# Kernel tuning notes

Measured on AMD Instinct MI355X. Metric: run time of the kernel, lower is better.

Reference implementation:

```python
import jax, jax.numpy as jnp
import numpy as np

B, N, C, T, K = 32, 4096, 768, 1000, 20

def setup_inputs() -> dict:
    key = jax.random.key(0)
    k1, k2, k3, k4 = jax.random.split(key, 4)
    g_feat = jax.random.normal(k1, (B, 1, C), dtype=jnp.float32)
    inp = jax.random.normal(k2, (B, N, C), dtype=jnp.float32)
    tau = jax.random.uniform(k3, (1,), dtype=jnp.float32)
    text_embeddings = jax.random.normal(k4, (T, C), dtype=jnp.float32) * 0.01
    return {"g_feat": g_feat, "input": inp, "tau": tau, "text_embeddings": text_embeddings}


def reference(g_feat, input, tau, text_embeddings):
    feat = input  # [B, N, C]
    # 1x1 conv of global feature against text embeddings -> class logits [B, T]
    vg_logit = jnp.einsum('bc,tc->bt', g_feat[:, 0, :], text_embeddings)
    # top-20 candidate categories per image
    _, indices = jax.lax.top_k(vg_logit, K)              # [B, K]
    agg_text_features = text_embeddings[indices]          # [B, K, C] gather
    # per-pixel logits against the 20 gathered text embeddings
    seg_logit = jnp.exp(tau[0]) * jnp.einsum('bkc,bnc->bkn', agg_text_features, feat)  # [B, K, N]
    # hard (straight-through) softmax over candidate axis (dim=-2)
    y_soft = jax.nn.softmax(seg_logit, axis=-2)
    idx = jnp.argmax(seg_logit, axis=-2)                  # [B, N]
    y_hard = jnp.moveaxis(jax.nn.one_hot(idx, K, dtype=seg_logit.dtype), -1, -2)  # [B, K, N]
    attn = y_hard - jax.lax.stop_gradient(y_soft) + y_soft
    # normalize over pixel axis (assign_eps = 1.0)
    assign_attn = attn / (jnp.sum(attn, axis=-1, keepdims=True) + 1.0)
    # combine: [B, N, K] @ [B, K, C] -> [B, N, C]
    text_grids = jnp.einsum('bkn,bkc->bnc', assign_attn, agg_text_features)
    return text_grids
```

## Files before the change

### kernel.cpp

```cpp
#include <hip/hip_runtime.h>
#include <cfloat>

#define B_ 32
#define N_ 4096
#define C_ 768
#define T_ 1000
#define K_ 20

#define PXB 256
#define PHC 32
#define NPH (C_/PHC)
#define GAP_TH 1e-4f
#define MAXF 16384

typedef float f32x4 __attribute__((ext_vector_type(4)));
typedef int   i32x4 __attribute__((ext_vector_type(4)));
typedef short s16x8 __attribute__((ext_vector_type(8)));

__device__ __forceinline__ unsigned short bf_rne(float x) {
    unsigned u = __float_as_uint(x);
    return (unsigned short)((u + 0x7fffu + ((u >> 16) & 1u)) >> 16);
}

__global__ __launch_bounds__(256) void k1_logits(const float* __restrict__ g_feat,
                                                 const float* __restrict__ text,
                                                 double* __restrict__ logits,
                                                 int* __restrict__ cnt,
                                                 int* __restrict__ flagcnt) {
    int b = blockIdx.x;
    int wid = threadIdx.x >> 6, lane = threadIdx.x & 63;
    int t = blockIdx.y * 4 + wid;
    if (b == 0 && blockIdx.y == 0) {
        for (int i = threadIdx.x; i < B_ * K_; i += 256) cnt[i] = 0;
        if (threadIdx.x == 0) flagcnt[0] = 0;
    }
    const float* g = g_feat + b * C_;
    const float* e = text + t * C_;
    double s = 0.0;
    #pragma unroll
    for (int j = 0; j < 12; ++j) {
        int c = lane + 64 * j;
        s += (double)g[c] * (double)e[c];
    }
    #pragma unroll
    for (int m = 32; m; m >>= 1) s += __shfl_xor(s, m);
    if (lane == 0) logits[b * T_ + t] = s;
}

__global__ __launch_bounds__(256) void k1b_topk(const double* __restrict__ logits,
                                                const float* __restrict__ text,
                                                float* __restrict__ agg,
                                                unsigned short* __restrict__ Ehi,
                                                unsigned short* __restrict__ Elo) {
    __shared__ int ssel[K_];
    int b = blockIdx.x, tid = threadIdx.x, lane = tid & 63;
    if (tid < 64) {
        double v[16];
        #pragma unroll
        for (int j = 0; j < 16; ++j) {
            int t = lane + 64 * j;
            v[j] = (t < T_) ? logits[b * T_ + t] : -DBL_MAX;
        }
        for (int it = 0; it < K_; ++it) {
            double bv = -DBL_MAX; int bi = 0x7fffffff;
            #pragma unroll
            for (int j = 0; j < 16; ++j) {
                int t = lane + 64 * j;
                if (v[j] > bv) { bv = v[j]; bi = t; }
            }
            #pragma unroll
            for (int m = 32; m; m >>= 1) {
                double ov = __shfl_xor(bv, m); int oi = __shfl_xor(bi, m);
                if (ov > bv || (ov == bv && oi < bi)) { bv = ov; bi = oi; }
            }
            if (lane == 0) ssel[it] = bi;
            #pragma unroll
            for (int j = 0; j < 16; ++j) {
                int t = lane + 64 * j;
                if (t == bi) v[j] = -DBL_MAX;
            }
        }
    }
    __syncthreads();
    for (int i = tid; i < K_ * C_; i += 256) {
        int j = i / C_, c = i - j * C_;
        agg[b * K_ * C_ + i] = text[ssel[j] * C_ + c];
    }
    for (int i = tid; i < 32 * C_; i += 256) {
        int r = i / C_, c = i - r * C_;
        float v = (r < K_) ? text[ssel[r] * C_ + c] : 0.f;
        unsigned u = __float_as_uint(v);
        float fh = __uint_as_float(u & 0xffff0000u);
        Ehi[(size_t)b * 32 * C_ + i] = (unsigned short)(u >> 16);
        Elo[(size_t)b * 32 * C_ + i] = bf_rne(v - fh);
    }
}

__global__ __launch_bounds__(256, 2) void k2_argmax(const float* __restrict__ feat,
                                                    const unsigned short* __restrict__ Ehi,
                                                    const unsigned short* __restrict__ Elo,
                                                    int* __restrict__ kidx,
                                                    int* __restrict__ cnt,
                                                    int* __restrict__ flagcnt,
                                                    int* __restrict__ flaglist) {
    __shared__ unsigned short hiT[2][PXB * PHC];
    __shared__ unsigned short loT[2][PXB * PHC];
    __shared__ int scnt[K_];
    int bx = blockIdx.x;
    int b = bx >> 4, tile = bx & 15;
    int n0 = tile * PXB;
    int tid = threadIdx.x, wid = tid >> 6, lane = tid & 63;
    if (tid < K_) scnt[tid] = 0;
    __syncthreads();

    const float* fb = feat + ((size_t)b * N_ + n0) * C_;
    const unsigned short* Eh = Ehi + (size_t)b * 32 * C_;
    const unsigned short* El = Elo + (size_t)b * 32 * C_;
    int r2 = (tid >> 1) & 3;
    int arow = lane & 15, acg = lane >> 4;

    f32x4 fr[8];
    auto LOADF = [&](int p) {
        const f32x4* fp_ = (const f32x4*)(fb + (size_t)tid * C_ + p * PHC);
        #pragma unroll
        for (int q = 0; q < 8; ++q) fr[q] = fp_[q ^ (2 * r2)];
    };
    auto CVTW = [&](int buf) {
        #pragma unroll
        for (int j = 0; j < 4; ++j) {
            unsigned hu[8], lu[8];
            #pragma unroll
            for (int m = 0; m < 8; ++m) {
                float x = (m < 4) ? fr[2 * j][m] : fr[2 * j + 1][m - 4];
                unsigned u = __float_as_uint(x);
                float fh = __uint_as_float(u & 0xffff0000u);
                hu[m] = u >> 16;
                lu[m] = bf_rne(x - fh);
            }
            int slot = tid * 4 + (j ^ r2);
            i32x4 hv = { (int)(hu[0] | (hu[1] << 16)), (int)(hu[2] | (hu[3] << 16)),
                         (int)(hu[4] | (hu[5] << 16)), (int)(hu[6] | (hu[7] << 16)) };
            i32x4 lv = { (int)(lu[0] | (lu[1] << 16)), (int)(lu[2] | (lu[3] << 16)),
                         (int)(lu[4] | (lu[5] << 16)), (int)(lu[6] | (lu[7] << 16)) };
            *(i32x4*)&hiT[buf][slot * 8] = hv;
            *(i32x4*)&loT[buf][slot * 8] = lv;
        }
    };

    s16x8 Ach0, Ach1, Acl0, Acl1, Anh0, Anh1, Anl0, Anl1;
    auto LOADA = [&](int p, s16x8& h0, s16x8& h1, s16x8& l0, s16x8& l1) {
        int co = p * PHC + acg * 8;
        h0 = *(const s16x8*)(Eh + (size_t)arow * C_ + co);
        h1 = *(const s16x8*)(Eh + (size_t)(16 + arow) * C_ + co);
        l0 = *(const s16x8*)(El + (size_t)arow * C_ + co);
        l1 = *(const s16x8*)(El + (size_t)(16 + arow) * C_ + co);
    };

    f32x4 acc0[4], acc1[4];
    #pragma unroll
    for (int i = 0; i < 4; ++i) { acc0[i] = (f32x4)0.f; acc1[i] = (f32x4)0.f; }

    LOADF(0);
    CVTW(0);
    LOADF(1);
    LOADA(0, Ach0, Ach1, Acl0, Acl1);
    LOADA(1, Anh0, Anh1, Anl0, Anl1);

    #pragma unroll 1
    for (int p = 0; p < NPH; ++p) {
        int cur = p & 1;
        if (p + 1 < NPH) {
            CVTW(cur ^ 1);
            if (p + 2 < NPH) LOADF(p + 2);
        }
        asm volatile("s_waitcnt lgkmcnt(0)" ::: "memory");
        __builtin_amdgcn_sched_barrier(0);

        #pragma unroll
        for (int i = 0; i < 4; ++i) {
            int slot = (wid * 64 + i * 16 + arow) * 4 + acg;
            s16x8 Bh = *(const s16x8*)&hiT[cur][slot * 8];
            s16x8 Bl = *(const s16x8*)&loT[cur][slot * 8];
            acc0[i] = __builtin_amdgcn_mfma_f32_16x16x32_bf16(Ach0, Bh, acc0[i], 0, 0, 0);
            acc1[i] = __builtin_amdgcn_mfma_f32_16x16x32_bf16(Ach1, Bh, acc1[i], 0, 0, 0);
            acc0[i] = __builtin_amdgcn_mfma_f32_16x16x32_bf16(Ach0, Bl, acc0[i], 0, 0, 0);
            acc1[i] = __builtin_amdgcn_mfma_f32_16x16x32_bf16(Ach1, Bl, acc1[i], 0, 0, 0);
            acc0[i] = __builtin_amdgcn_mfma_f32_16x16x32_bf16(Acl0, Bh, acc0[i], 0, 0, 0);
            acc1[i] = __builtin_amdgcn_mfma_f32_16x16x32_bf16(Acl1, Bh, acc1[i], 0, 0, 0);
        }

        Ach0 = Anh0; Ach1 = Anh1; Acl0 = Anl0; Acl1 = Anl1;
        if (p + 2 < NPH) LOADA(p + 2, Anh0, Anh1, Anl0, Anl1);
    }

    #pragma unroll
    for (int i = 0; i < 4; ++i) {
        int kb = acg * 4;
        float m1 = acc0[i][0]; int i1 = kb; float m2 = -FLT_MAX;
        #pragma unroll
        for (int r = 1; r < 4; ++r) {
            float v = acc0[i][r];
            if (v > m1) { m2 = m1; m1 = v; i1 = kb + r; }
            else if (v > m2) m2 = v;
        }
        if (acg == 0) {
            #pragma unroll
            for (int r = 0; r < 4; ++r) {
                float v = acc1[i][r];
                if (v > m1) { m2 = m1; m1 = v; i1 = 16 + r; }
                else if (v > m2) m2 = v;
            }
        }
        #pragma unroll
        for (int s = 16; s < 64; s <<= 1) {
            float om1 = __shfl_xor(m1, s); int oi1 = __shfl_xor(i1, s);
            float om2 = __shfl_xor(m2, s);
            if (om1 > m1 || (om1 == m1 && oi1 < i1)) { m2 = fmaxf(m1, om2); m1 = om1; i1 = oi1; }
            else { m2 = fmaxf(m2, om1); }
        }
        if (lane < 16) {
            int n = n0 + wid * 64 + i * 16 + lane;
            kidx[b * N_ + n] = i1;
            atomicAdd(&scnt[i1], 1);
            if (m1 - m2 < GAP_TH) {
                int pos = atomicAdd(flagcnt, 1);
                if (pos < MAXF) flaglist[pos] = b * N_ + n;
            }
        }
    }
    __syncthreads();
    if (tid < K_) atomicAdd(&cnt[b * K_ + tid], scnt[tid]);
}

__global__ __launch_bounds__(256) void k25_refine(const float* __restrict__ feat,
                                                  const float* __restrict__ agg,
                                                  int* __restrict__ kidx,
                                                  int* __restrict__ cnt,
                                                  const int* __restrict__ flagcnt,
                                                  const int* __restrict__ flaglist) {
    int wid = threadIdx.x >> 6, lane = threadIdx.x & 63;
    int wg = blockIdx.x * 4 + wid;
    int nf = flagcnt[0]; if (nf > MAXF) nf = MAXF;
    for (int e = wg; e < nf; e += gridDim.x * 4) {
        int pix = flaglist[e];
        int b = pix >> 12;
        const float* fr = feat + (size_t)pix * C_;
        const float* ebase = agg + b * K_ * C_;
        double fd[12];
        #pragma unroll
        for (int j = 0; j < 12; ++j) fd[j] = (double)fr[lane + 64 * j];
        double best = -DBL_MAX; int bi = 0;
        for (int k = 0; k < K_; ++k) {
            const float* er = ebase + k * C_;
            double s = 0.0;
            #pragma unroll
            for (int j = 0; j < 12; ++j) s += fd[j] * (double)er[lane + 64 * j];
            #pragma unroll
            for (int m = 32; m; m >>= 1) s += __shfl_xor(s, m);
            if (s > best) { best = s; bi = k; }
        }
        if (lane == 0) {
            int old = kidx[pix];
            if (old != bi) {
                kidx[pix] = bi;
                atomicSub(&cnt[b * K_ + old], 1);
                atomicAdd(&cnt[b * K_ + bi], 1);
            }
        }
    }
}

__global__ __launch_bounds__(256) void k3s_scale(const float* __restrict__ agg,
                                                 const int* __restrict__ cnt,
                                                 float* __restrict__ sagg) {
    __shared__ float sc[K_];
    int b = blockIdx.x, tid = threadIdx.x;
    if (tid < K_) sc[tid] = 1.0f / ((float)cnt[b * K_ + tid] + 1.0f);
    __syncthreads();
    const f32x4* a4 = (const f32x4*)(agg + (size_t)b * K_ * C_);
    f32x4* s4 = (f32x4*)(sagg + (size_t)b * K_ * C_);
    #pragma unroll 1
    for (int i = tid; i < K_ * (C_ / 4); i += 256) {
        int k = i / (C_ / 4);
        s4[i] = a4[i] * sc[k];
    }
}

__global__ __launch_bounds__(256) void k4_out(const float* __restrict__ sagg,
                                              const int* __restrict__ kidx,
                                              float* __restrict__ out) {
    int wid = threadIdx.x >> 6, lane = threadIdx.x & 63;
    int wg = blockIdx.x * 4 + wid;
    int base = wg * 8;
    int b = base >> 12;
    int kk[8];
    #pragma unroll
    for (int i = 0; i < 8; ++i) kk[i] = kidx[base + i];
    const f32x4* sagg4 = (const f32x4*)sagg;
    f32x4* out4 = (f32x4*)out;

    f32x4 va0, va1, va2, vb0, vb1, vb2;
    {
        const f32x4* a4 = sagg4 + (size_t)(b * K_ + kk[0]) * (C_ / 4);
        va0 = a4[lane]; va1 = a4[lane + 64]; va2 = a4[lane + 128];
    }
    #pragma unroll
    for (int i = 0; i < 8; ++i) {
        if (i + 1 < 8) {
            const f32x4* a4 = sagg4 + (size_t)(b * K_ + kk[i + 1]) * (C_ / 4);
            vb0 = a4[lane]; vb1 = a4[lane + 64]; vb2 = a4[lane + 128];
        }
        f32x4* o4 = out4 + (size_t)(base + i) * (C_ / 4);
        o4[lane] = va0; o4[lane + 64] = va1; o4[lane + 128] = va2;
        va0 = vb0; va1 = vb1; va2 = vb2;
    }
}

extern "C" void kernel_launch(void* const* d_in, const int* in_sizes, int n_in,
                              void* d_out, int out_size, void* d_ws, size_t ws_size,
                              hipStream_t stream) {
    const float* g_feat = (const float*)d_in[0];
    const float* feat   = (const float*)d_in[1];
    const float* text   = (const float*)d_in[3];
    float* out = (float*)d_out;

    char* ws = (char*)d_ws;
    double* logits        = (double*)(ws + 0);
    float*  agg           = (float*) (ws + 262144);
    int*    cnt           = (int*)   (ws + 2230784);
    int*    flagc         = (int*)   (ws + 2233344);
    int*    flagl         = (int*)   (ws + 2233408);
    int*    kidx          = (int*)   (ws + 2301504);
    unsigned short* Ehi   = (unsigned short*)(ws + 2825792);
    unsigned short* Elo   = (unsigned short*)(ws + 4398656);
    float*  sagg          = (float*) (ws + 5971520);

    k1_logits<<<dim3(32, 250), 256, 0, stream>>>(g_feat, text, logits, cnt, flagc);
    k1b_topk<<<32, 256, 0, stream>>>(logits, text, agg, Ehi, Elo);
    k2_argmax<<<32 * 16, 256, 0, stream>>>(feat, Ehi, Elo, kidx, cnt, flagc, flagl);
    k25_refine<<<1024, 256, 0, stream>>>(feat, agg, kidx, cnt, flagc, flagl);
    k3s_scale<<<32, 256, 0, stream>>>(agg, cnt, sagg);
    k4_out<<<4096, 256, 0, stream>>>(sagg, kidx, out);
}
```

Measured before the change: 281.5 us.

## Coalesce feature loads and pre-pack text fragments in MFMA lane order

In the argmax kernel, feature loads change from one thread per pixel row (strided by C) to eight lanes cooperatively reading contiguous 128-byte chunks of a row, so global reads coalesce. The LDS tile layout changes to an XOR-swizzled row-major layout to match. The top-k kernel now stages the hi/lo bf16 split in shared memory and writes it out pre-packed in MFMA operand order, so each A-fragment load is one contiguous vector per lane. It also folds the agg copy into the same loop. The cost is a large static LDS buffer in k1b (~96KB) and more work in that single-block-per-batch kernel.

```diff
diff --git a/kernel.cpp b/kernel.cpp
--- a/kernel.cpp
+++ b/kernel.cpp
@@ -14,7 +14,7 @@
 #define MAXF 16384
 
 typedef float f32x4 __attribute__((ext_vector_type(4)));
-typedef int   i32x4 __attribute__((ext_vector_type(4)));
+typedef int   i32x2 __attribute__((ext_vector_type(2)));
 typedef short s16x8 __attribute__((ext_vector_type(8)));
 
 __device__ __forceinline__ unsigned short bf_rne(float x) {
@@ -50,8 +50,9 @@
 __global__ __launch_bounds__(256) void k1b_topk(const double* __restrict__ logits,
                                                 const float* __restrict__ text,
                                                 float* __restrict__ agg,
-                                                unsigned short* __restrict__ Ehi,
-                                                unsigned short* __restrict__ Elo) {
+                                                unsigned short* __restrict__ Epk) {
+    __shared__ unsigned short hiL[32 * C_];
+    __shared__ unsigned short loL[32 * C_];
     __shared__ int ssel[K_];
     int b = blockIdx.x, tid = threadIdx.x, lane = tid & 63;
     if (tid < 64) {
@@ -82,23 +83,27 @@
         }
     }
     __syncthreads();
-    for (int i = tid; i < K_ * C_; i += 256) {
-        int j = i / C_, c = i - j * C_;
-        agg[b * K_ * C_ + i] = text[ssel[j] * C_ + c];
-    }
     for (int i = tid; i < 32 * C_; i += 256) {
         int r = i / C_, c = i - r * C_;
         float v = (r < K_) ? text[ssel[r] * C_ + c] : 0.f;
+        if (r < K_) agg[b * K_ * C_ + i] = v;
         unsigned u = __float_as_uint(v);
         float fh = __uint_as_float(u & 0xffff0000u);
-        Ehi[(size_t)b * 32 * C_ + i] = (unsigned short)(u >> 16);
-        Elo[(size_t)b * 32 * C_ + i] = bf_rne(v - fh);
+        hiL[i] = (unsigned short)(u >> 16);
+        loL[i] = bf_rne(v - fh);
+    }
+    __syncthreads();
+    for (int i = tid; i < 24 * 256; i += 256) {
+        int p = i >> 8, r = i & 255, f = r >> 6, ln = r & 63;
+        int row = (f & 1) * 16 + (ln & 15);
+        int col = p * 32 + (ln >> 4) * 8;
+        const unsigned short* src = ((f < 2) ? hiL : loL) + row * C_ + col;
+        *(s16x8*)(Epk + ((size_t)b * 6144 + i) * 8) = *(const s16x8*)src;
     }
 }
 
 __global__ __launch_bounds__(256, 2) void k2_argmax(const float* __restrict__ feat,
-                                                    const unsigned short* __restrict__ Ehi,
-                                                    const unsigned short* __restrict__ Elo,
+                                                    const unsigned short* __restrict__ Epk,
                                                     int* __restrict__ kidx,
                                                     int* __restrict__ cnt,
                                                     int* __restrict__ flagcnt,
@@ -114,46 +119,47 @@
     __syncthreads();
 
     const float* fb = feat + ((size_t)b * N_ + n0) * C_;
-    const unsigned short* Eh = Ehi + (size_t)b * 32 * C_;
-    const unsigned short* El = Elo + (size_t)b * 32 * C_;
-    int r2 = (tid >> 1) & 3;
+    const unsigned short* Eb = Epk + (size_t)b * 6144 * 8;
+    int l3 = lane >> 3;
+    int ch = lane & 7;
     int arow = lane & 15, acg = lane >> 4;
 
     f32x4 fr[8];
     auto LOADF = [&](int p) {
-        const f32x4* fp_ = (const f32x4*)(fb + (size_t)tid * C_ + p * PHC);
-        #pragma unroll
-        for (int q = 0; q < 8; ++q) fr[q] = fp_[q ^ (2 * r2)];
+        #pragma unroll
+        for (int i = 0; i < 8; ++i) {
+            int row = wid * 64 + i * 8 + l3;
+            fr[i] = *(const f32x4*)(fb + (size_t)row * C_ + p * PHC + ch * 4);
+        }
     };
     auto CVTW = [&](int buf) {
-        #pragma unroll
-        for (int j = 0; j < 4; ++j) {
-            unsigned hu[8], lu[8];
-            #pragma unroll
-            for (int m = 0; m < 8; ++m) {
-                float x = (m < 4) ? fr[2 * j][m] : fr[2 * j + 1][m - 4];
-                unsigned u = __float_as_uint(x);
-                float fh = __uint_as_float(u & 0xffff0000u);
-                hu[m] = u >> 16;
-                lu[m] = bf_rne(x - fh);
-            }
-            int slot = tid * 4 + (j ^ r2);
-            i32x4 hv = { (int)(hu[0] | (hu[1] << 16)), (int)(hu[2] | (hu[3] << 16)),
-                         (int)(hu[4] | (hu[5] << 16)), (int)(hu[6] | (hu[7] << 16)) };
-            i32x4 lv = { (int)(lu[0] | (lu[1] << 16)), (int)(lu[2] | (lu[3] << 16)),
-                         (int)(lu[4] | (lu[5] << 16)), (int)(lu[6] | (lu[7] << 16)) };
-            *(i32x4*)&hiT[buf][slot * 8] = hv;
-            *(i32x4*)&loT[buf][slot * 8] = lv;
+        int g = ch >> 1, h = ch & 1;
+        #pragma unroll
+        for (int i = 0; i < 8; ++i) {
+            int row = wid * 64 + i * 8 + l3;
+            unsigned u0 = __float_as_uint(fr[i].x), u1 = __float_as_uint(fr[i].y);
+            unsigned u2 = __float_as_uint(fr[i].z), u3 = __float_as_uint(fr[i].w);
+            unsigned ha = (u0 >> 16) | (u1 & 0xffff0000u);
+            unsigned hb = (u2 >> 16) | (u3 & 0xffff0000u);
+            unsigned la = (unsigned)bf_rne(fr[i].x - __uint_as_float(u0 & 0xffff0000u)) |
+                          ((unsigned)bf_rne(fr[i].y - __uint_as_float(u1 & 0xffff0000u)) << 16);
+            unsigned lb = (unsigned)bf_rne(fr[i].z - __uint_as_float(u2 & 0xffff0000u)) |
+                          ((unsigned)bf_rne(fr[i].w - __uint_as_float(u3 & 0xffff0000u)) << 16);
+            int a16 = row * PHC + ((g ^ (row & 3)) * 8) + h * 4;
+            i32x2 hv = { (int)ha, (int)hb };
+            i32x2 lv = { (int)la, (int)lb };
+            *(i32x2*)&hiT[buf][a16] = hv;
+            *(i32x2*)&loT[buf][a16] = lv;
         }
     };
 
     s16x8 Ach0, Ach1, Acl0, Acl1, Anh0, Anh1, Anl0, Anl1;
     auto LOADA = [&](int p, s16x8& h0, s16x8& h1, s16x8& l0, s16x8& l1) {
-        int co = p * PHC + acg * 8;
-        h0 = *(const s16x8*)(Eh + (size_t)arow * C_ + co);
-        h1 = *(const s16x8*)(Eh + (size_t)(16 + arow) * C_ + co);
-        l0 = *(const s16x8*)(El + (size_t)arow * C_ + co);
-        l1 = *(const s16x8*)(El + (size_t)(16 + arow) * C_ + co);
+        const s16x8* ap = (const s16x8*)(Eb + (size_t)p * 256 * 8);
+        h0 = ap[0 * 64 + lane];
+        h1 = ap[1 * 64 + lane];
+        l0 = ap[2 * 64 + lane];
+        l1 = ap[3 * 64 + lane];
     };
 
     f32x4 acc0[4], acc1[4];
@@ -178,9 +184,10 @@
 
         #pragma unroll
         for (int i = 0; i < 4; ++i) {
-            int slot = (wid * 64 + i * 16 + arow) * 4 + acg;
-            s16x8 Bh = *(const s16x8*)&hiT[cur][slot * 8];
-            s16x8 Bl = *(const s16x8*)&loT[cur][slot * 8];
+            int px = wid * 64 + i * 16 + arow;
+            int a16 = px * PHC + (acg ^ (px & 3)) * 8;
+            s16x8 Bh = *(const s16x8*)&hiT[cur][a16];
+            s16x8 Bl = *(const s16x8*)&loT[cur][a16];
             acc0[i] = __builtin_amdgcn_mfma_f32_16x16x32_bf16(Ach0, Bh, acc0[i], 0, 0, 0);
             acc1[i] = __builtin_amdgcn_mfma_f32_16x16x32_bf16(Ach1, Bh, acc1[i], 0, 0, 0);
             acc0[i] = __builtin_amdgcn_mfma_f32_16x16x32_bf16(Ach0, Bl, acc0[i], 0, 0, 0);
@@ -331,13 +338,12 @@
     int*    flagc         = (int*)   (ws + 2233344);
     int*    flagl         = (int*)   (ws + 2233408);
     int*    kidx          = (int*)   (ws + 2301504);
-    unsigned short* Ehi   = (unsigned short*)(ws + 2825792);
-    unsigned short* Elo   = (unsigned short*)(ws + 4398656);
+    unsigned short* Epk   = (unsigned short*)(ws + 2825792);
     float*  sagg          = (float*) (ws + 5971520);
 
     k1_logits<<<dim3(32, 250), 256, 0, stream>>>(g_feat, text, logits, cnt, flagc);
-    k1b_topk<<<32, 256, 0, stream>>>(logits, text, agg, Ehi, Elo);
-    k2_argmax<<<32 * 16, 256, 0, stream>>>(feat, Ehi, Elo, kidx, cnt, flagc, flagl);
+    k1b_topk<<<32, 256, 0, stream>>>(logits, text, agg, Epk);
+    k2_argmax<<<32 * 16, 256, 0, stream>>>(feat, Epk, kidx, cnt, flagc, flagl);
     k25_refine<<<1024, 256, 0, stream>>>(feat, agg, kidx, cnt, flagc, flagl);
     k3s_scale<<<32, 256, 0, stream>>>(agg, cnt, sagg);
     k4_out<<<4096, 256, 0, stream>>>(sagg, kidx, out);
```

Measured after the change: 273.0 us. 1.03x faster.
